# Optimization experiments

Measured on AMD Instinct MI355X. Metric: run time of the kernel, lower is better.

Reference implementation:

```python
import jax, jax.numpy as jnp
import numpy as np

B, CIN, COUT, H, W, K, S = 32, 16, 32, 14, 14, 5, 2


def _conv(x, w, stride, groups=1):
    # x: [N, Cin_g*groups, H, W], w: [Cout, Cin_g, K, K], VALID padding, no bias
    return jax.lax.conv_general_dilated(
        x, w, (stride, stride), 'VALID',
        dimension_numbers=('NCHW', 'OIHW', 'NCHW'),
        feature_group_count=groups)


def setup_inputs() -> dict:
    key = jax.random.key(0)
    k1, k2, k3 = jax.random.split(key, 3)
    u = jax.random.normal(k1, (B, CIN, H, W), jnp.float32)
    C = jax.random.normal(k2, (B, CIN, H, W, H, W), jnp.float32)
    # per-output-channel single-channel kernels, as in Conv2d(1,1,K) list
    w = jax.random.normal(k3, (COUT, 1, K, K), jnp.float32) * (1.0 / K)
    return {"u": u, "C": C, "w": w}


def reference(u, C, w):
    b, cin, h, wd = u.shape
    cout = w.shape[0]
    # ---- mean path: conv each input channel with every kernel, sum over Cin ----
    m = _conv(u.reshape(b * cin, 1, h, wd), w, S)          # [b*cin, cout, OH, OW]
    oh, ow = m.shape[2], m.shape[3]
    out_mean = m.reshape(b, cin, cout, oh, ow).sum(axis=1)  # [b, cout, OH, OW]

    # ---- covariance path: apply the same conv to both spatial index pairs ----
    # conv over original dims (4,5)
    t = _conv(C.reshape(b * cin * h * wd, 1, h, wd), w, S)  # [b*cin*h*w, cout, OH, OW]
    t = t.reshape(b, cin, h, wd, cout, oh, ow)
    # bring original dims (2,3) to conv position; keep kernel index as channel
    t = t.transpose(0, 1, 5, 6, 4, 2, 3)                    # [b, cin, OH, OW, cout, h, w]
    t = t.reshape(b * cin * oh * ow, cout, h, wd)
    # grouped conv: channel i convolved with kernel i (second application)
    t = _conv(t, w, S, groups=cout)                         # [b*cin*OH*OW, cout, OH, OW]
    t = t.reshape(b, cin, oh, ow, cout, oh, ow)             # [b,c,oh45,ow45,i,oh23,ow23]
    # torch output layout: [b, i, oh23, ow23, oh45, ow45], summed over cin
    out_cov = t.transpose(0, 4, 5, 6, 2, 3, 1).sum(axis=-1)
    return (out_mean, out_cov)
```

## Files before the change

kernel.cpp:

```cpp
#include <hip/hip_runtime.h>


#define NB   32
#define NCIN 16
#define NCO  32
#define HH   14
#define OO   5
#define HW   196
#define T1_PER_BI 4900

__device__ float g_T1[NB * NCO * T1_PER_BI];

__global__ __launch_bounds__(448) void k1_reduce_conv(const float* __restrict__ C,
                                                      const float* __restrict__ w) {
  const int blk = blockIdx.x;
  const int b   = blk / HH;
  const int h1  = blk % HH;
  const int tid = threadIdx.x;

  __shared__ float wl[NCO * 25];
  __shared__ float cs[14 * 224];
  __shared__ float t1s[448 * 25];

  for (int t = tid; t < NCO * 25; t += 448) wl[t] = w[t];

  const float4* C4 = (const float4*)C;
  const int base4 = ((b * NCIN) * HH + h1) * 686;
  for (int j4 = tid; j4 < 686; j4 += 448) {
    float4 acc = make_float4(0.f, 0.f, 0.f, 0.f);
    #pragma unroll
    for (int c = 0; c < NCIN; ++c) {
      float4 v = C4[base4 + c * 9604 + j4];
      acc.x += v.x; acc.y += v.y; acc.z += v.z; acc.w += v.w;
    }
    const float vv[4] = {acc.x, acc.y, acc.z, acc.w};
    const int j = j4 * 4;
    #pragma unroll
    for (int e = 0; e < 4; ++e) {
      const int jj = j + e;
      const int w1 = jj / 196, rem = jj % 196;
      const int h2 = rem / 14, w2 = rem % 14;
      cs[w1 * 224 + h2 * 16 + w2] = vv[e];
    }
  }
  __syncthreads();

  const int i  = tid & 31;
  const int w1 = tid >> 5;
  float wr[25];
  #pragma unroll
  for (int t = 0; t < 25; ++t) wr[t] = wl[i * 25 + t];

  float acc[25];
  #pragma unroll
  for (int t = 0; t < 25; ++t) acc[t] = 0.f;

  #pragma unroll
  for (int r = 0; r < 5; ++r) {
    #pragma unroll
    for (int cc = 0; cc < 5; ++cc) {
      const int row = 2 * r + cc;
      const float4* rp = (const float4*)(cs + w1 * 224 + row * 16);
      float4 x0 = rp[0], x1 = rp[1], x2 = rp[2], x3 = rp[3];
      const float col[16] = {x0.x, x0.y, x0.z, x0.w,
                             x1.x, x1.y, x1.z, x1.w,
                             x2.x, x2.y, x2.z, x2.w,
                             x3.x, x3.y, x3.z, x3.w};
      #pragma unroll
      for (int s = 0; s < 5; ++s) {
        #pragma unroll
        for (int d = 0; d < 5; ++d)
          acc[r * 5 + s] += wr[cc * 5 + d] * col[2 * s + d];
      }
    }
  }

  #pragma unroll
  for (int t = 0; t < 25; ++t) t1s[i * 350 + w1 * 25 + t] = acc[t];
  __syncthreads();

  const size_t gbase = (size_t)b * NCO * T1_PER_BI + (size_t)h1 * 350;
  for (int idx = tid; idx < 11200; idx += 448) {
    const int i2 = idx / 350, rem = idx % 350;
    g_T1[gbase + (size_t)i2 * T1_PER_BI + rem] = t1s[idx];
  }
}

__global__ __launch_bounds__(128) void k2_out(const float* __restrict__ u,
                                              const float* __restrict__ w,
                                              float* __restrict__ out) {
  const int blk = blockIdx.x;
  const int tid = threadIdx.x;

  if (blk < NB * NCO) {
    __shared__ float sl[T1_PER_BI];
    const float4* src = (const float4*)(g_T1 + (size_t)blk * T1_PER_BI);
    float4* sl4 = (float4*)sl;
    for (int j = tid; j < 1225; j += 128) sl4[j] = src[j];

    const int i = blk & 31;
    float wr[25];
    #pragma unroll
    for (int t = 0; t < 25; ++t) wr[t] = w[i * 25 + t];
    __syncthreads();

    for (int o = tid; o < 625; o += 128) {
      const int p  = o / 125;
      const int q  = (o / 25) % 5;
      const int rs = o % 25;
      float acc = 0.f;
      #pragma unroll
      for (int a = 0; a < 5; ++a) {
        #pragma unroll
        for (int bb = 0; bb < 5; ++bb)
          acc += wr[a * 5 + bb] * sl[((2 * p + a) * 14 + (2 * q + bb)) * 25 + rs];
      }
      out[25600 + blk * 625 + o] = acc;
    }
  } else {
    const int b = blk - NB * NCO;
    __shared__ float us[HW];
    for (int j = tid; j < HW; j += 128) {
      float acc = 0.f;
      #pragma unroll
      for (int c = 0; c < NCIN; ++c) acc += u[(b * NCIN + c) * HW + j];
      us[j] = acc;
    }
    __syncthreads();
    for (int o = tid; o < NCO * 25; o += 128) {
      const int i = o / 25;
      const int p = (o / 5) % 5;
      const int q = o % 5;
      float acc = 0.f;
      #pragma unroll
      for (int a = 0; a < 5; ++a) {
        #pragma unroll
        for (int bb = 0; bb < 5; ++bb)
          acc += w[i * 25 + a * 5 + bb] * us[(2 * p + a) * 14 + 2 * q + bb];
      }
      out[b * 800 + o] = acc;
    }
  }
}

extern "C" void kernel_launch(void* const* d_in, const int* in_sizes, int n_in,
                              void* d_out, int out_size, void* d_ws, size_t ws_size,
                              hipStream_t stream) {
  const float* u = (const float*)d_in[0];
  const float* C = (const float*)d_in[1];
  const float* w = (const float*)d_in[2];
  float* out = (float*)d_out;

  hipLaunchKernelGGL(k1_reduce_conv, dim3(NB * HH), dim3(448), 0, stream, C, w);
  hipLaunchKernelGGL(k2_out, dim3(NB * NCO + NB), dim3(128), 0, stream, u, w, out);
}
```

Baseline: 136.2 us.

## Move first conv pass into output kernel, reduce C over Cin in a separate pass

The first kernel now only sums C over input channels and writes the reduced tensor (rows h1 0..12 only) to a global buffer. The second kernel, one block per (batch, output channel), stages each h1 slab in shared memory, computes the first conv into a shared T1 tile, then applies the second conv. This drops the large g_T1 intermediate write and read, but every block of a batch re-reads the same reduced slab (32x redundant loads) and runs the first conv with a serial 13-step loop and many syncs.

New measurement: 141.7 us. 1.04x slower.

```diff
diff --git a/kernel.cpp b/kernel.cpp
--- a/kernel.cpp
+++ b/kernel.cpp
@@ -5,106 +5,71 @@
 #define NCIN 16
 #define NCO  32
 #define HH   14
-#define OO   5
 #define HW   196
-#define T1_PER_BI 4900
+#define CS_B 9604
+#define CS_B13 8918
 
-__device__ float g_T1[NB * NCO * T1_PER_BI];
+__device__ float g_CS[NB * 38416];
 
-__global__ __launch_bounds__(448) void k1_reduce_conv(const float* __restrict__ C,
-                                                      const float* __restrict__ w) {
-  const int blk = blockIdx.x;
-  const int b   = blk / HH;
-  const int h1  = blk % HH;
-  const int tid = threadIdx.x;
-
-  __shared__ float wl[NCO * 25];
-  __shared__ float cs[14 * 224];
-  __shared__ float t1s[448 * 25];
-
-  for (int t = tid; t < NCO * 25; t += 448) wl[t] = w[t];
-
+__global__ __launch_bounds__(256) void k1_cs(const float* __restrict__ C) {
+  const int b    = blockIdx.y;
+  const int idx4 = blockIdx.x * 256 + threadIdx.x;
+  if (idx4 >= CS_B13) return;
   const float4* C4 = (const float4*)C;
-  const int base4 = ((b * NCIN) * HH + h1) * 686;
-  for (int j4 = tid; j4 < 686; j4 += 448) {
-    float4 acc = make_float4(0.f, 0.f, 0.f, 0.f);
-    #pragma unroll
-    for (int c = 0; c < NCIN; ++c) {
-      float4 v = C4[base4 + c * 9604 + j4];
-      acc.x += v.x; acc.y += v.y; acc.z += v.z; acc.w += v.w;
-    }
-    const float vv[4] = {acc.x, acc.y, acc.z, acc.w};
-    const int j = j4 * 4;
-    #pragma unroll
-    for (int e = 0; e < 4; ++e) {
-      const int jj = j + e;
-      const int w1 = jj / 196, rem = jj % 196;
-      const int h2 = rem / 14, w2 = rem % 14;
-      cs[w1 * 224 + h2 * 16 + w2] = vv[e];
-    }
+  float4* CS4 = (float4*)g_CS;
+  const int base = (b * NCIN) * CS_B + idx4;
+  float4 acc = make_float4(0.f, 0.f, 0.f, 0.f);
+  #pragma unroll
+  for (int c = 0; c < NCIN; ++c) {
+    float4 v = C4[base + c * CS_B];
+    acc.x += v.x; acc.y += v.y; acc.z += v.z; acc.w += v.w;
   }
-  __syncthreads();
-
-  const int i  = tid & 31;
-  const int w1 = tid >> 5;
-  float wr[25];
-  #pragma unroll
-  for (int t = 0; t < 25; ++t) wr[t] = wl[i * 25 + t];
-
-  float acc[25];
-  #pragma unroll
-  for (int t = 0; t < 25; ++t) acc[t] = 0.f;
-
-  #pragma unroll
-  for (int r = 0; r < 5; ++r) {
-    #pragma unroll
-    for (int cc = 0; cc < 5; ++cc) {
-      const int row = 2 * r + cc;
-      const float4* rp = (const float4*)(cs + w1 * 224 + row * 16);
-      float4 x0 = rp[0], x1 = rp[1], x2 = rp[2], x3 = rp[3];
-      const float col[16] = {x0.x, x0.y, x0.z, x0.w,
-                             x1.x, x1.y, x1.z, x1.w,
-                             x2.x, x2.y, x2.z, x2.w,
-                             x3.x, x3.y, x3.z, x3.w};
-      #pragma unroll
-      for (int s = 0; s < 5; ++s) {
-        #pragma unroll
-        for (int d = 0; d < 5; ++d)
-          acc[r * 5 + s] += wr[cc * 5 + d] * col[2 * s + d];
-      }
-    }
-  }
-
-  #pragma unroll
-  for (int t = 0; t < 25; ++t) t1s[i * 350 + w1 * 25 + t] = acc[t];
-  __syncthreads();
-
-  const size_t gbase = (size_t)b * NCO * T1_PER_BI + (size_t)h1 * 350;
-  for (int idx = tid; idx < 11200; idx += 448) {
-    const int i2 = idx / 350, rem = idx % 350;
-    g_T1[gbase + (size_t)i2 * T1_PER_BI + rem] = t1s[idx];
-  }
+  CS4[b * CS_B + idx4] = acc;
 }
 
-__global__ __launch_bounds__(128) void k2_out(const float* __restrict__ u,
+__global__ __launch_bounds__(256) void k2_out(const float* __restrict__ u,
                                               const float* __restrict__ w,
                                               float* __restrict__ out) {
   const int blk = blockIdx.x;
   const int tid = threadIdx.x;
 
   if (blk < NB * NCO) {
-    __shared__ float sl[T1_PER_BI];
-    const float4* src = (const float4*)(g_T1 + (size_t)blk * T1_PER_BI);
-    float4* sl4 = (float4*)sl;
-    for (int j = tid; j < 1225; j += 128) sl4[j] = src[j];
+    const int b = blk >> 5;
+    const int i = blk & 31;
 
-    const int i = blk & 31;
+    __shared__ float slab[2744];
+    __shared__ float T1[4900];
+
     float wr[25];
     #pragma unroll
     for (int t = 0; t < 25; ++t) wr[t] = w[i * 25 + t];
+
+    const float4* CS4 = (const float4*)g_CS;
+    float4* slab4 = (float4*)slab;
+
+    for (int h1 = 0; h1 < 13; ++h1) {
+      __syncthreads();
+      for (int j = tid; j < 686; j += 256)
+        slab4[j] = CS4[b * CS_B + h1 * 686 + j];
+      __syncthreads();
+      for (int o = tid; o < 325; o += 256) {
+        const int w1 = o / 25;
+        const int rs = o % 25;
+        const int r = rs / 5, s = rs % 5;
+        const float* p0 = slab + w1 * 196 + (2 * r) * 14 + 2 * s;
+        float acc = 0.f;
+        #pragma unroll
+        for (int cc = 0; cc < 5; ++cc) {
+          #pragma unroll
+          for (int d = 0; d < 5; ++d)
+            acc += wr[cc * 5 + d] * p0[cc * 14 + d];
+        }
+        T1[h1 * 350 + w1 * 25 + rs] = acc;
+      }
+    }
     __syncthreads();
 
-    for (int o = tid; o < 625; o += 128) {
+    for (int o = tid; o < 625; o += 256) {
       const int p  = o / 125;
       const int q  = (o / 25) % 5;
       const int rs = o % 25;
@@ -113,21 +78,21 @@
       for (int a = 0; a < 5; ++a) {
         #pragma unroll
         for (int bb = 0; bb < 5; ++bb)
-          acc += wr[a * 5 + bb] * sl[((2 * p + a) * 14 + (2 * q + bb)) * 25 + rs];
+          acc += wr[a * 5 + bb] * T1[(2 * p + a) * 350 + (2 * q + bb) * 25 + rs];
       }
       out[25600 + blk * 625 + o] = acc;
     }
   } else {
     const int b = blk - NB * NCO;
     __shared__ float us[HW];
-    for (int j = tid; j < HW; j += 128) {
+    for (int j = tid; j < HW; j += 256) {
       float acc = 0.f;
       #pragma unroll
       for (int c = 0; c < NCIN; ++c) acc += u[(b * NCIN + c) * HW + j];
       us[j] = acc;
     }
     __syncthreads();
-    for (int o = tid; o < NCO * 25; o += 128) {
+    for (int o = tid; o < NCO * 25; o += 256) {
       const int i = o / 25;
       const int p = (o / 5) % 5;
       const int q = o % 5;
@@ -151,6 +116,6 @@
   const float* w = (const float*)d_in[2];
   float* out = (float*)d_out;
 
-  hipLaunchKernelGGL(k1_reduce_conv, dim3(NB * HH), dim3(448), 0, stream, C, w);
-  hipLaunchKernelGGL(k2_out, dim3(NB * NCO + NB), dim3(128), 0, stream, u, w, out);
+  hipLaunchKernelGGL(k1_cs, dim3(35, 32), dim3(256), 0, stream, C);
+  hipLaunchKernelGGL(k2_out, dim3(NB * NCO + NB), dim3(256), 0, stream, u, w, out);
 }
```
